# Optimization experiments

Measured on AMD Instinct MI355X. Metric: run time of the kernel, lower is better.

The kernel has to match this reference:

```python
import jax, jax.numpy as jnp
import numpy as np

BIT_W = 8   # config.bit_wt
BIT_A = 8   # config.bit_act (activations sliced 2 bits at a time)
STRIDE = (1, 1)
PAD = 1


def _conv(a, w):
    # NCHW input, OIHW weight, stride 1, symmetric padding 1 (matches wrapped Conv2d)
    return jax.lax.conv_general_dilated(
        a, w, window_strides=STRIDE, padding=[(PAD, PAD), (PAD, PAD)],
        dimension_numbers=("NCHW", "OIHW", "NCHW"))


def setup_inputs() -> dict:
    key = jax.random.key(0)
    k1, k2, k3 = jax.random.split(key, 3)
    x = jax.random.normal(k1, (64, 64, 56, 56), dtype=jnp.float32)
    weight = jax.random.normal(k2, (64, 64, 3, 3), dtype=jnp.float32)
    bias = jax.random.normal(k3, (64,), dtype=jnp.float32)
    scale_a = jnp.full((1,), 20.0, dtype=jnp.float32)      # conv_q.scale
    scale_w = jnp.full((1,), 20.0, dtype=jnp.float32)      # wrapped_module.weight_scale
    zero_point = jnp.full((1,), -128.0, dtype=jnp.float32)  # conv_q.zero_point
    return {"x": x, "weight": weight, "bias": bias,
            "scale_a": scale_a, "scale_w": scale_w, "zero_point": zero_point}


def reference(x, weight, bias, scale_a, scale_w, zero_point):
    sa = scale_a[0]
    sw = scale_w[0]
    zp = zero_point[0]
    # activation quantization: round(x*scale_a - zero_point), clamp to [0, 2^bit_act - 1]
    q_in = jnp.clip(jnp.round(x * sa - zp), 0.0, 2.0 ** BIT_A - 1.0)
    # weight quantization: round(w * scale_w), interpreted in two's complement
    q_w = jnp.round(weight * sw)
    w_off = q_w + 2.0 ** BIT_W  # (w + (1 << bit_weight)) before bit masking

    acc = jnp.zeros((), dtype=jnp.float32)
    for ba in range(BIT_A // 2):
        # 2-bit activation slice: (a >> 2*ba) & 3
        a_sl = jnp.mod(jnp.floor(q_in / (4.0 ** ba)), 4.0)
        for bw in range(BIT_W):
            # weight bit bw: ((w + 2^B) >> bw) & 1
            w_bit = jnp.mod(jnp.floor(w_off / (2.0 ** bw)), 2.0)
            r = _conv(a_sl, w_bit)
            sgn = -1.0 if bw == BIT_W - 1 else 1.0  # MSB = sign bit (two's complement)
            acc = acc + sgn * (2.0 ** (2 * ba + bw)) * r

    # zero-point correction: conv(ones * zp, q_w) added back (no-op when zp == 0)
    acc = acc + zp * _conv(jnp.ones_like(q_in), q_w)

    out = acc / (sw * sa) + bias[None, :, None, None]
    return out
```

## Files before the change

### kernel.cpp

```cpp
#include <hip/hip_runtime.h>


typedef int v4i __attribute__((ext_vector_type(4)));

__global__ __launch_bounds__(64) void prep_wq(const float* __restrict__ wt,
                                              const float* __restrict__ sw_p,
                                              const float* __restrict__ zp_p,
                                              signed char* __restrict__ w8,
                                              float* __restrict__ corr_tab) {
  const int o = blockIdx.x;
  const int i = threadIdx.x;
  const float sw = sw_p[0];
  const float* wp = wt + (size_t)(o * 64 + i) * 9;
  int q[9];
#pragma unroll
  for (int k = 0; k < 9; ++k) q[k] = (int)rintf(wp[k] * sw);
#pragma unroll
  for (int k = 0; k < 9; ++k)
    w8[(o * 9 + k) * 64 + i] = (signed char)(q[k] & 255);

  int stc[9], srw[9];
#pragma unroll
  for (int k = 0; k < 9; ++k) {
    int a = (int)(signed char)(q[k] & 255);
    int b = q[k];
#pragma unroll
    for (int off = 32; off; off >>= 1) {
      a += __shfl_xor(a, off);
      b += __shfl_xor(b, off);
    }
    stc[k] = a; srw[k] = b;
  }
  const float zp = zp_p[0];
  if (i < 9) {
    const int v = i / 3, hc = i % 3;
    float corr = 0.0f;
#pragma unroll
    for (int k = 0; k < 9; ++k) {
      const int kh = k / 3, kw = k % 3;
      const bool drop = (v == 1 && kh == 0) || (v == 2 && kh == 2) ||
                        (hc == 1 && kw == 0) || (hc == 2 && kw == 2);
      if (!drop) corr += 128.0f * (float)stc[k] + zp * (float)srw[k];
    }
    corr_tab[i * 64 + o] = corr;
  }
}

__global__ __launch_bounds__(256, 4) void conv_fused(
    const float* __restrict__ x, const signed char* __restrict__ w8,
    const float* __restrict__ corr_tab, const float* __restrict__ bias,
    const float* __restrict__ sa_p, const float* __restrict__ sw_p,
    const float* __restrict__ zp_p, float* __restrict__ out) {
  __shared__ __align__(16) signed char lds[32192];
  signed char* const trbuf = lds + 24576;

  const int tid = threadIdx.x;
  const int n = blockIdx.y;
  const int h0 = blockIdx.x * 4;
  const float sa = sa_p[0], zp = zp_p[0];
  const float* xim = x + (size_t)n * 200704;

#pragma unroll 1
  for (int p = 0; p < 3; ++p) {
    const int ihb = h0 - 1 + 2 * p;
#pragma unroll
    for (int it = 0; it < 7; ++it) {
      const int idx = tid + 256 * it;
      const int r = idx >= 896;
      const int rem = idx - 896 * r;
      const int c = (rem * 2341) >> 15;
      const int w4 = rem - c * 14;
      const int ih = ihb + r;
      const bool valid = (unsigned)ih < 56u;
      float4 v = make_float4(0.0f, 0.0f, 0.0f, 0.0f);
      if (valid)
        v = *(const float4*)(xim + (size_t)c * 3136 + ih * 56 + w4 * 4);
      signed char* dst = trbuf + r * 3808 + w4 * 272 + c;
      const float vv[4] = {v.x, v.y, v.z, v.w};
#pragma unroll
      for (int e = 0; e < 4; ++e) {
        signed char b = 0;
        if (valid) {
          float tq;
          {
#pragma clang fp contract(off)
            tq = vv[e] * sa - zp;
          }
          float qf = rintf(tq);
          qf = fminf(fmaxf(qf, 0.0f), 255.0f);
          b = (signed char)((int)qf - 128);
        }
        dst[e * 68] = b;
      }
    }
    __syncthreads();
    const int cnt = p ? 464 : 608;
#pragma unroll
    for (int it = 0; it < 3; ++it) {
      const int idx = tid + 256 * it;
      if (idx < 448) {
        const int r = idx >= 224;
        const int u = idx - 224 * r;
        const int w = u >> 2, q2 = u & 3;
        const unsigned* s = (const unsigned*)(trbuf + r * 3808 + w * 68 + q2 * 16);
        const uint4 vv = make_uint4(s[0], s[1], s[2], s[3]);
        *((uint4*)(lds + ((2 * p + r) * 58 + w + 1) * 64 + q2 * 16)) = vv;
      } else if (idx < 464) {
        const int p2 = idx - 448;
        const int r = p2 >> 3;
        const int side = (p2 >> 2) & 1;
        const int j = p2 & 3;
        *((uint4*)(lds + ((2 * p + r) * 58 + side * 57) * 64 + j * 16)) =
            make_uint4(0, 0, 0, 0);
      } else if (idx < cnt) {
        ((uint4*)(lds + 22272))[idx - 464] = ((const uint4*)corr_tab)[idx - 464];
      }
    }
    __syncthreads();
  }

  const int lane = tid & 63;
  const int wv = tid >> 6;
  const int phalf = wv & 1;
  const int ogp = wv >> 1;
  const int ln = lane & 15;
  const int kg = lane >> 4;
  const int oa = ogp * 32 + ln;

  const signed char* wba = w8 + (size_t)oa * 576 + kg * 16;
  v4i Ba[9], Bb[9];
#pragma unroll
  for (int t = 0; t < 9; ++t) {
    Ba[t] = *(const v4i*)(wba + t * 64);
    Bb[t] = *(const v4i*)(wba + 9216 + t * 64);
  }

  const float sw = sw_p[0];
  const float rden = 1.0f / (sw * sa);
  const float boa = bias[oa], bob = bias[oa + 16];
  const float* ctab = (const float*)(lds + 22272);
  const float cFa = ctab[oa];
  const float cFb = ctab[oa + 16];
  float* const outa = out + (size_t)(n * 64 + oa) * 3136 + h0 * 56;
  float* const outb = outa + 16 * 3136;

#pragma unroll 1
  for (int t = 0; t < 7; ++t) {
    const int pb = phalf * 112 + t * 16;
    const int pa = pb + ln;
    const int hr = (pa * 9363) >> 19;
    const int wc = pa - hr * 56;
    const signed char* ab = lds + (hr * 58 + wc) * 64 + kg * 16;
    v4i acca = {0, 0, 0, 0}, accb = {0, 0, 0, 0};
#pragma unroll
    for (int kh = 0; kh < 3; ++kh) {
#pragma unroll
      for (int kw = 0; kw < 3; ++kw) {
        const v4i A = *(const v4i*)(ab + (kh * 58 + kw) * 64);
        acca = __builtin_amdgcn_mfma_i32_16x16x64_i8(A, Ba[kh * 3 + kw], acca, 0, 0, 0);
        accb = __builtin_amdgcn_mfma_i32_16x16x64_i8(A, Bb[kh * 3 + kw], accb, 0, 0, 0);
      }
    }
    const int pxb = pb + kg * 4;
    float ta[4], tb[4];
#pragma unroll
    for (int e = 0; e < 4; ++e) {
      const int px = pxb + e;
      const int hh = (px * 9363) >> 19;
      const int ww = px - hh * 56;
      const int hg = h0 + hh;
      float ca = cFa, cb = cFb;
      if ((hg == 0) | (hg == 55) | (ww == 0) | (ww == 55)) {
        const int vcase = (hg == 0) ? 1 : ((hg == 55) ? 2 : 0);
        const int hcase = (ww == 0) ? 1 : ((ww == 55) ? 2 : 0);
        const int cidx = (vcase * 3 + hcase) * 64;
        ca = ctab[cidx + oa];
        cb = ctab[cidx + oa + 16];
      }
      ta[e] = ((float)acca[e] + ca) * rden + boa;
      tb[e] = ((float)accb[e] + cb) * rden + bob;
    }
    *(float4*)(outa + pxb) = make_float4(ta[0], ta[1], ta[2], ta[3]);
    *(float4*)(outb + pxb) = make_float4(tb[0], tb[1], tb[2], tb[3]);
  }
}

extern "C" void kernel_launch(void* const* d_in, const int* in_sizes, int n_in,
                              void* d_out, int out_size, void* d_ws, size_t ws_size,
                              hipStream_t stream) {
  const float* x    = (const float*)d_in[0];
  const float* wt   = (const float*)d_in[1];
  const float* bias = (const float*)d_in[2];
  const float* sa   = (const float*)d_in[3];
  const float* sw   = (const float*)d_in[4];
  const float* zp   = (const float*)d_in[5];
  float* out = (float*)d_out;

  char* ws = (char*)d_ws;
  signed char* w8 = (signed char*)ws;
  float* corr_tab = (float*)(ws + 36864);

  prep_wq<<<64, 64, 0, stream>>>(wt, sw, zp, w8, corr_tab);
  conv_fused<<<dim3(14, 64), 256, 0, stream>>>(x, w8, corr_tab, bias, sa, sw, zp, out);
}
```

Measured before the change: 128.4 us.

## Quantize activations directly into padded-row LDS layout, dropping transpose staging

Each thread now loads four channels per pixel group and packs their quantized bytes into one 32-bit word. It writes that word straight into the final LDS image, whose pixel stride is padded from 64 to 80 bytes to reduce bank conflicts. This removes the three-phase loop with an intermediate transpose buffer, its extra LDS pass, and five of the six barriers. The correction table is read from global memory instead of being staged in LDS, which adds a few scattered global reads in the epilogue. The padded stride changes the address pattern of the MFMA operand reads.

```diff
diff --git a/kernel.cpp b/kernel.cpp
--- a/kernel.cpp
+++ b/kernel.cpp
@@ -2,6 +2,8 @@
 
 
 typedef int v4i __attribute__((ext_vector_type(4)));
+
+#define ROWB 80
 
 __global__ __launch_bounds__(64) void prep_wq(const float* __restrict__ wt,
                                               const float* __restrict__ sw_p,
@@ -51,73 +53,59 @@
     const float* __restrict__ corr_tab, const float* __restrict__ bias,
     const float* __restrict__ sa_p, const float* __restrict__ sw_p,
     const float* __restrict__ zp_p, float* __restrict__ out) {
-  __shared__ __align__(16) signed char lds[32192];
-  signed char* const trbuf = lds + 24576;
-
+  __shared__ __align__(16) signed char lds[6 * 58 * ROWB];
   const int tid = threadIdx.x;
   const int n = blockIdx.y;
   const int h0 = blockIdx.x * 4;
   const float sa = sa_p[0], zp = zp_p[0];
   const float* xim = x + (size_t)n * 200704;
 
-#pragma unroll 1
-  for (int p = 0; p < 3; ++p) {
-    const int ihb = h0 - 1 + 2 * p;
+#pragma unroll 2
+  for (int it = 0; it < 6; ++it) {
+    const int idx = tid + 256 * it;
+    if (idx < 1344) {
+      const int cg = idx & 15;
+      const int rem = idx >> 4;
+      const int row = (rem * 2341) >> 15;
+      const int w4 = rem - row * 14;
+      const int ih = h0 - 1 + row;
+      const bool valid = (unsigned)ih < 56u;
+      int* const dst = (int*)lds + (row * 58 + w4 * 4 + 1) * (ROWB / 4) + cg;
+      if (valid) {
+        float4 v[4];
 #pragma unroll
-    for (int it = 0; it < 7; ++it) {
-      const int idx = tid + 256 * it;
-      const int r = idx >= 896;
-      const int rem = idx - 896 * r;
-      const int c = (rem * 2341) >> 15;
-      const int w4 = rem - c * 14;
-      const int ih = ihb + r;
-      const bool valid = (unsigned)ih < 56u;
-      float4 v = make_float4(0.0f, 0.0f, 0.0f, 0.0f);
-      if (valid)
-        v = *(const float4*)(xim + (size_t)c * 3136 + ih * 56 + w4 * 4);
-      signed char* dst = trbuf + r * 3808 + w4 * 272 + c;
-      const float vv[4] = {v.x, v.y, v.z, v.w};
+        for (int j = 0; j < 4; ++j)
+          v[j] = *(const float4*)(xim + (size_t)(cg * 4 + j) * 3136 + ih * 56 + w4 * 4);
 #pragma unroll
-      for (int e = 0; e < 4; ++e) {
-        signed char b = 0;
-        if (valid) {
-          float tq;
-          {
+        for (int e = 0; e < 4; ++e) {
+          int dw = 0;
+#pragma unroll
+          for (int j = 0; j < 4; ++j) {
+            const float xv = (&v[j].x)[e];
+            float tq;
+            {
 #pragma clang fp contract(off)
-            tq = vv[e] * sa - zp;
+              tq = xv * sa - zp;
+            }
+            float qf = rintf(tq);
+            qf = fminf(fmaxf(qf, 0.0f), 255.0f);
+            const int b = ((int)qf - 128) & 255;
+            dw |= b << (8 * j);
           }
-          float qf = rintf(tq);
-          qf = fminf(fmaxf(qf, 0.0f), 255.0f);
-          b = (signed char)((int)qf - 128);
+          dst[e * (ROWB / 4)] = dw;
         }
-        dst[e * 68] = b;
+      } else {
+#pragma unroll
+        for (int e = 0; e < 4; ++e) dst[e * (ROWB / 4)] = 0;
       }
+    } else {
+      const int z = idx - 1344;
+      const int loc = z >> 4, d = z & 15;
+      const int row = loc >> 1, side = loc & 1;
+      ((int*)lds)[(row * 58 + side * 57) * (ROWB / 4) + d] = 0;
     }
-    __syncthreads();
-    const int cnt = p ? 464 : 608;
-#pragma unroll
-    for (int it = 0; it < 3; ++it) {
-      const int idx = tid + 256 * it;
-      if (idx < 448) {
-        const int r = idx >= 224;
-        const int u = idx - 224 * r;
-        const int w = u >> 2, q2 = u & 3;
-        const unsigned* s = (const unsigned*)(trbuf + r * 3808 + w * 68 + q2 * 16);
-        const uint4 vv = make_uint4(s[0], s[1], s[2], s[3]);
-        *((uint4*)(lds + ((2 * p + r) * 58 + w + 1) * 64 + q2 * 16)) = vv;
-      } else if (idx < 464) {
-        const int p2 = idx - 448;
-        const int r = p2 >> 3;
-        const int side = (p2 >> 2) & 1;
-        const int j = p2 & 3;
-        *((uint4*)(lds + ((2 * p + r) * 58 + side * 57) * 64 + j * 16)) =
-            make_uint4(0, 0, 0, 0);
-      } else if (idx < cnt) {
-        ((uint4*)(lds + 22272))[idx - 464] = ((const uint4*)corr_tab)[idx - 464];
-      }
-    }
-    __syncthreads();
   }
+  __syncthreads();
 
   const int lane = tid & 63;
   const int wv = tid >> 6;
@@ -138,9 +126,8 @@
   const float sw = sw_p[0];
   const float rden = 1.0f / (sw * sa);
   const float boa = bias[oa], bob = bias[oa + 16];
-  const float* ctab = (const float*)(lds + 22272);
-  const float cFa = ctab[oa];
-  const float cFb = ctab[oa + 16];
+  const float cFa = corr_tab[oa];
+  const float cFb = corr_tab[oa + 16];
   float* const outa = out + (size_t)(n * 64 + oa) * 3136 + h0 * 56;
   float* const outb = outa + 16 * 3136;
 
@@ -150,13 +137,13 @@
     const int pa = pb + ln;
     const int hr = (pa * 9363) >> 19;
     const int wc = pa - hr * 56;
-    const signed char* ab = lds + (hr * 58 + wc) * 64 + kg * 16;
+    const signed char* ab = lds + (hr * 58 + wc) * ROWB + kg * 16;
     v4i acca = {0, 0, 0, 0}, accb = {0, 0, 0, 0};
 #pragma unroll
     for (int kh = 0; kh < 3; ++kh) {
 #pragma unroll
       for (int kw = 0; kw < 3; ++kw) {
-        const v4i A = *(const v4i*)(ab + (kh * 58 + kw) * 64);
+        const v4i A = *(const v4i*)(ab + (kh * 58 + kw) * ROWB);
         acca = __builtin_amdgcn_mfma_i32_16x16x64_i8(A, Ba[kh * 3 + kw], acca, 0, 0, 0);
         accb = __builtin_amdgcn_mfma_i32_16x16x64_i8(A, Bb[kh * 3 + kw], accb, 0, 0, 0);
       }
@@ -174,8 +161,8 @@
         const int vcase = (hg == 0) ? 1 : ((hg == 55) ? 2 : 0);
         const int hcase = (ww == 0) ? 1 : ((ww == 55) ? 2 : 0);
         const int cidx = (vcase * 3 + hcase) * 64;
-        ca = ctab[cidx + oa];
-        cb = ctab[cidx + oa + 16];
+        ca = corr_tab[cidx + oa];
+        cb = corr_tab[cidx + oa + 16];
       }
       ta[e] = ((float)acca[e] + ca) * rden + boa;
       tb[e] = ((float)accb[e] + cb) * rden + bob;
```

Measured after the change: 125.4 us, median of 2. -2.4%, faster.
